# Kernel tuning notes

Measured on AMD Instinct MI355X. Metric: run time of the kernel, lower is better.

Reference implementation:

```python
import jax, jax.numpy as jnp
import numpy as np

ALPHA = 0.0005
TAU = 0.2


def setup_inputs() -> dict:
    key = jax.random.key(0)
    k1, k2, k3 = jax.random.split(key, 3)
    output = jax.random.normal(k1, (8192, 1000), dtype=jnp.float32)
    target = jax.random.normal(k2, (8192, 1000), dtype=jnp.float32)
    conv_w = jax.random.normal(k3, (256, 256, 128, 3), dtype=jnp.float32)
    return {"output": output, "target": target, "conv_w": conv_w}


def reference(output, target, conv_w):
    # base loss (nn.MSELoss with default 'mean' reduction)
    loss = jnp.mean((output - target) ** 2)

    # Diversity regularizer: pairwise cosine similarity between slices
    # conv_w[:, :, i, :] along dim 2 ('filters' = size(2) in the original).
    F = conv_w.shape[2]
    # V: [F, D] with D = out_ch * in_ch * kw
    V = jnp.transpose(conv_w, (2, 0, 1, 3)).reshape(F, -1)
    norms = jnp.linalg.norm(V, axis=1)                      # [F]
    G = (V @ V.T) / (norms[:, None] * norms[None, :])       # [F, F] cosine Gram

    # keep entries with tau < sim <= 1 and i != j
    offdiag = ~jnp.eye(F, dtype=bool)
    mask = (G > TAU) & (G <= 1.0) & offdiag
    reg = jnp.sum(jnp.where(mask, G, jnp.zeros((), dtype=G.dtype)))

    return loss + ALPHA * reg
```

## Files before the change

### kernel.cpp

```cpp
#include <hip/hip_runtime.h>
#include <hip/hip_bf16.h>


typedef __attribute__((ext_vector_type(8))) short bf16x8;
typedef __attribute__((ext_vector_type(4))) float f32x4;

#define ALPHA 0.0005f
#define TAU 0.2f

#define FDIM 128
#define TSTRIDE_DW 52
#define GRAM_NBLK 512
#define CHUNK_F4 3072
#define GRAM_ELEMS (FDIM * FDIM)
#define MSE_N4 2048000
#define MSE_NBLK 2048

__device__ __forceinline__ unsigned int pack_bf2(float lo, float hi) {
    union { float f; unsigned int u; } a, b;
    a.f = lo; b.f = hi;
    unsigned int al = (a.u + 0x7fffu + ((a.u >> 16) & 1u)) >> 16;
    unsigned int bh = (b.u + 0x7fffu + ((b.u >> 16) & 1u)) & 0xffff0000u;
    return (al & 0xffffu) | bh;
}

__global__ void __launch_bounds__(256) mse_kernel(
        const float* __restrict__ o, const float* __restrict__ t,
        float* __restrict__ mse_part) {
    __shared__ float red[4];
    const int tid = threadIdx.x;
    const float4* o4 = reinterpret_cast<const float4*>(o);
    const float4* t4 = reinterpret_cast<const float4*>(t);
    float s = 0.f;
    for (int i = blockIdx.x * 256 + tid; i < MSE_N4; i += MSE_NBLK * 256) {
        float4 a = o4[i], b = t4[i];
        float dx = a.x - b.x, dy = a.y - b.y, dz = a.z - b.z, dw = a.w - b.w;
        s += dx * dx + dy * dy + dz * dz + dw * dw;
    }
    for (int off = 32; off; off >>= 1) s += __shfl_down(s, off);
    if ((tid & 63) == 0) red[tid >> 6] = s;
    __syncthreads();
    if (tid == 0) mse_part[blockIdx.x] = red[0] + red[1] + red[2] + red[3];
}

__device__ __forceinline__ void loadc(const f32x4* __restrict__ src4,
                                      size_t base4, f32x4 (&R)[12]) {
#pragma unroll
    for (int it = 0; it < 6; ++it) {
        R[2 * it]     = src4[base4 + 16 * it];
        R[2 * it + 1] = src4[base4 + 96 + 16 * it];
    }
}

__device__ __forceinline__ void convertc(const f32x4 (&R)[12],
                                         unsigned int* __restrict__ tb,
                                         int p, int q) {
#pragma unroll
    for (int it = 0; it < 6; ++it)
#pragma unroll
        for (int u = 0; u < 4; ++u) {
            const int idx = (q + 16 * it) * 4 + u;
            const int f = idx / 3;
            const int k = idx - 3 * f;
            tb[f * TSTRIDE_DW + k * 16 + p] = pack_bf2(R[2 * it][u], R[2 * it + 1][u]);
        }
}

__device__ __forceinline__ void barrier_tile() {
    asm volatile("s_waitcnt lgkmcnt(0)" ::: "memory");
    __builtin_amdgcn_sched_barrier(0);
    __builtin_amdgcn_s_barrier();
    __builtin_amdgcn_sched_barrier(0);
}

__device__ __forceinline__ void mfmaph(const unsigned short* __restrict__ tu,
                                       int wave, int colr, int hi8,
                                       f32x4 (&acc0)[8], f32x4 (&acc1)[8]) {
#pragma unroll
    for (int ks = 0; ks < 3; ++ks) {
        const int koff = ks * 32 + hi8;
        bf16x8 a0 = *reinterpret_cast<const bf16x8*>(
            &tu[(wave * 32 + colr) * (TSTRIDE_DW * 2) + koff]);
        bf16x8 a1 = *reinterpret_cast<const bf16x8*>(
            &tu[(wave * 32 + 16 + colr) * (TSTRIDE_DW * 2) + koff]);
#pragma unroll
        for (int cc = 0; cc < 8; ++cc) {
            bf16x8 b = *reinterpret_cast<const bf16x8*>(
                &tu[(cc * 16 + colr) * (TSTRIDE_DW * 2) + koff]);
            acc0[cc] = __builtin_amdgcn_mfma_f32_16x16x32_bf16(a0, b, acc0[cc], 0, 0, 0);
            acc1[cc] = __builtin_amdgcn_mfma_f32_16x16x32_bf16(a1, b, acc1[cc], 0, 0, 0);
        }
    }
}

template <int ATOMIC>
__global__ void __launch_bounds__(256, 2) gram_kernel(
        const float* __restrict__ conv, float* __restrict__ out) {
    __shared__ unsigned int tile[2][FDIM * TSTRIDE_DW];
    const int tid = threadIdx.x;
    const int lane = tid & 63;
    const int wave = tid >> 6;
    const int p = tid >> 4;
    const int q = tid & 15;
    const int colr = lane & 15;
    const int hi8 = (lane >> 4) * 8;
    const unsigned short* t0u = reinterpret_cast<const unsigned short*>(tile[0]);
    const unsigned short* t1u = reinterpret_cast<const unsigned short*>(tile[1]);

    f32x4 acc0[8], acc1[8];
#pragma unroll
    for (int cc = 0; cc < 8; ++cc) { acc0[cc] = (f32x4)0.f; acc1[cc] = (f32x4)0.f; }

    const f32x4* src4 = reinterpret_cast<const f32x4*>(conv);
    const size_t cb = (size_t)blockIdx.x * (4 * CHUNK_F4) + (2 * p) * 96 + q;

    f32x4 RA[12], RB[12];
    loadc(src4, cb + 0 * CHUNK_F4, RA);

    loadc(src4, cb + 1 * CHUNK_F4, RB);
    convertc(RA, tile[0], p, q);
    barrier_tile();
    mfmaph(t0u, wave, colr, hi8, acc0, acc1);
    loadc(src4, cb + 2 * CHUNK_F4, RA);
    convertc(RB, tile[1], p, q);
    barrier_tile();
    mfmaph(t1u, wave, colr, hi8, acc0, acc1);
    loadc(src4, cb + 3 * CHUNK_F4, RB);
    convertc(RA, tile[0], p, q);
    barrier_tile();
    mfmaph(t0u, wave, colr, hi8, acc0, acc1);
    convertc(RB, tile[1], p, q);
    barrier_tile();
    mfmaph(t1u, wave, colr, hi8, acc0, acc1);

    float* my = ATOMIC ? out : out + (size_t)blockIdx.x * GRAM_ELEMS;
    const int rsub = (lane >> 4) << 2;
#pragma unroll
    for (int cc = 0; cc < 8; ++cc) {
        const int col = cc * 16 + colr;
#pragma unroll
        for (int j = 0; j < 4; ++j) {
            const int r0 = wave * 32 + rsub + j;
            if (ATOMIC) {
                atomicAdd(&my[r0 * FDIM + col], acc0[cc][j]);
                atomicAdd(&my[(r0 + 16) * FDIM + col], acc1[cc][j]);
            } else {
                my[r0 * FDIM + col] = acc0[cc][j];
                my[(r0 + 16) * FDIM + col] = acc1[cc][j];
            }
        }
    }
}

__global__ void __launch_bounds__(256) reduce_kernel(
        const float* __restrict__ partials, float* __restrict__ gram) {
    __shared__ float acc_s[64][5];
    const int tid = threadIdx.x;
    const int el = tid & 63;
    const int sl = tid >> 6;
    const int e = blockIdx.x * 64 + el;
    float s = 0.f;
#pragma unroll 16
    for (int b = sl * 128; b < sl * 128 + 128; ++b)
        s += partials[(size_t)b * GRAM_ELEMS + e];
    acc_s[el][sl] = s;
    __syncthreads();
    if (tid < 64)
        gram[blockIdx.x * 64 + tid] =
            acc_s[tid][0] + acc_s[tid][1] + acc_s[tid][2] + acc_s[tid][3];
}

__global__ void __launch_bounds__(256) finalize_kernel(
        const float* __restrict__ gram, const float* __restrict__ mse_part,
        float* __restrict__ out) {
    __shared__ float rn[FDIM];
    __shared__ float red[4];
    __shared__ float redm[4];
    const int tid = threadIdx.x;
    if (tid < FDIM) rn[tid] = rsqrtf(gram[tid * (FDIM + 1)]);
    __syncthreads();
    float s = 0.f;
    for (int i = tid; i < GRAM_ELEMS; i += 256) {
        const int row = i >> 7, col = i & 127;
        const float g = gram[i] * rn[row] * rn[col];
        if (row != col && g > TAU && g <= 1.0f) s += g;
    }
    float m = 0.f;
#pragma unroll 8
    for (int j = 0; j < 8; ++j) m += mse_part[tid * 8 + j];
    for (int off = 32; off; off >>= 1) {
        s += __shfl_down(s, off);
        m += __shfl_down(m, off);
    }
    if ((tid & 63) == 0) { red[tid >> 6] = s; redm[tid >> 6] = m; }
    __syncthreads();
    if (tid == 0)
        out[0] = (redm[0] + redm[1] + redm[2] + redm[3]) * (1.0f / 8192000.0f) +
                 ALPHA * (red[0] + red[1] + red[2] + red[3]);
}

extern "C" void kernel_launch(void* const* d_in, const int* in_sizes, int n_in,
                              void* d_out, int out_size, void* d_ws, size_t ws_size,
                              hipStream_t stream) {
    const float* output = (const float*)d_in[0];
    const float* target = (const float*)d_in[1];
    const float* conv   = (const float*)d_in[2];
    float* out = (float*)d_out;

    float* wsf      = (float*)d_ws;
    float* mse_part = wsf;
    float* gram     = wsf + MSE_NBLK;
    float* partials = wsf + MSE_NBLK + GRAM_ELEMS;

    const size_t need =
        (MSE_NBLK + GRAM_ELEMS + (size_t)GRAM_NBLK * GRAM_ELEMS) * sizeof(float);

    if (ws_size >= need) {
        gram_kernel<0><<<GRAM_NBLK, 256, 0, stream>>>(conv, partials);
        mse_kernel<<<MSE_NBLK, 256, 0, stream>>>(output, target, mse_part);
        reduce_kernel<<<GRAM_ELEMS / 64, 256, 0, stream>>>(partials, gram);
    } else {
        hipMemsetAsync(gram, 0, GRAM_ELEMS * sizeof(float), stream);
        gram_kernel<1><<<GRAM_NBLK, 256, 0, stream>>>(conv, gram);
        mse_kernel<<<MSE_NBLK, 256, 0, stream>>>(output, target, mse_part);
    }
    finalize_kernel<<<1, 256, 0, stream>>>(gram, mse_part, out);
}
```

Before: 62.03 us.

## Store Gram partials as packed bf16 pairs to halve partial traffic

Each Gram block now packs its 512 partial 128x128 tiles into bf16 pairs (two rows per 32-bit word) instead of full fp32, halving the partial write and reduce read volume. The reduce kernel unpacks and sums the pairs, and finalize remaps indices to the new packed layout. A sched_barrier is added after the global loads, and the atomic fallback path and workspace size check are removed. This adds rounding error to each partial and assumes a large enough workspace.

```diff
diff --git a/kernel.cpp b/kernel.cpp
--- a/kernel.cpp
+++ b/kernel.cpp
@@ -9,10 +9,11 @@
 #define TAU 0.2f
 
 #define FDIM 128
-#define TSTRIDE_DW 52
+#define TSTRIDE 52
 #define GRAM_NBLK 512
 #define CHUNK_F4 3072
-#define GRAM_ELEMS (FDIM * FDIM)
+#define GRAM_ELEMS 16384
+#define NPAIRQ 8192
 #define MSE_N4 2048000
 #define MSE_NBLK 2048
 
@@ -50,6 +51,7 @@
         R[2 * it]     = src4[base4 + 16 * it];
         R[2 * it + 1] = src4[base4 + 96 + 16 * it];
     }
+    __builtin_amdgcn_sched_barrier(0);
 }
 
 __device__ __forceinline__ void convertc(const f32x4 (&R)[12],
@@ -62,7 +64,7 @@
             const int idx = (q + 16 * it) * 4 + u;
             const int f = idx / 3;
             const int k = idx - 3 * f;
-            tb[f * TSTRIDE_DW + k * 16 + p] = pack_bf2(R[2 * it][u], R[2 * it + 1][u]);
+            tb[f * TSTRIDE + k * 16 + p] = pack_bf2(R[2 * it][u], R[2 * it + 1][u]);
         }
 }
 
@@ -80,23 +82,22 @@
     for (int ks = 0; ks < 3; ++ks) {
         const int koff = ks * 32 + hi8;
         bf16x8 a0 = *reinterpret_cast<const bf16x8*>(
-            &tu[(wave * 32 + colr) * (TSTRIDE_DW * 2) + koff]);
+            &tu[(wave * 32 + colr) * (TSTRIDE * 2) + koff]);
         bf16x8 a1 = *reinterpret_cast<const bf16x8*>(
-            &tu[(wave * 32 + 16 + colr) * (TSTRIDE_DW * 2) + koff]);
+            &tu[(wave * 32 + 16 + colr) * (TSTRIDE * 2) + koff]);
 #pragma unroll
         for (int cc = 0; cc < 8; ++cc) {
             bf16x8 b = *reinterpret_cast<const bf16x8*>(
-                &tu[(cc * 16 + colr) * (TSTRIDE_DW * 2) + koff]);
+                &tu[(cc * 16 + colr) * (TSTRIDE * 2) + koff]);
             acc0[cc] = __builtin_amdgcn_mfma_f32_16x16x32_bf16(a0, b, acc0[cc], 0, 0, 0);
             acc1[cc] = __builtin_amdgcn_mfma_f32_16x16x32_bf16(a1, b, acc1[cc], 0, 0, 0);
         }
     }
 }
 
-template <int ATOMIC>
 __global__ void __launch_bounds__(256, 2) gram_kernel(
-        const float* __restrict__ conv, float* __restrict__ out) {
-    __shared__ unsigned int tile[2][FDIM * TSTRIDE_DW];
+        const float* __restrict__ conv, unsigned int* __restrict__ pp) {
+    __shared__ unsigned int tile[2][FDIM * TSTRIDE];
     const int tid = threadIdx.x;
     const int lane = tid & 63;
     const int wave = tid >> 6;
@@ -133,55 +134,64 @@
     barrier_tile();
     mfmaph(t1u, wave, colr, hi8, acc0, acc1);
 
-    float* my = ATOMIC ? out : out + (size_t)blockIdx.x * GRAM_ELEMS;
+    unsigned int* myp = pp + (size_t)blockIdx.x * NPAIRQ;
     const int rsub = (lane >> 4) << 2;
 #pragma unroll
     for (int cc = 0; cc < 8; ++cc) {
         const int col = cc * 16 + colr;
 #pragma unroll
         for (int j = 0; j < 4; ++j) {
-            const int r0 = wave * 32 + rsub + j;
-            if (ATOMIC) {
-                atomicAdd(&my[r0 * FDIM + col], acc0[cc][j]);
-                atomicAdd(&my[(r0 + 16) * FDIM + col], acc1[cc][j]);
-            } else {
-                my[r0 * FDIM + col] = acc0[cc][j];
-                my[(r0 + 16) * FDIM + col] = acc1[cc][j];
-            }
+            const int pr = wave * 16 + rsub + j;
+            myp[pr * FDIM + col] = pack_bf2(acc0[cc][j], acc1[cc][j]);
         }
     }
 }
 
 __global__ void __launch_bounds__(256) reduce_kernel(
-        const float* __restrict__ partials, float* __restrict__ gram) {
-    __shared__ float acc_s[64][5];
-    const int tid = threadIdx.x;
-    const int el = tid & 63;
-    const int sl = tid >> 6;
-    const int e = blockIdx.x * 64 + el;
-    float s = 0.f;
-#pragma unroll 16
-    for (int b = sl * 128; b < sl * 128 + 128; ++b)
-        s += partials[(size_t)b * GRAM_ELEMS + e];
-    acc_s[el][sl] = s;
-    __syncthreads();
-    if (tid < 64)
-        gram[blockIdx.x * 64 + tid] =
-            acc_s[tid][0] + acc_s[tid][1] + acc_s[tid][2] + acc_s[tid][3];
+        const unsigned int* __restrict__ pp, float* __restrict__ gram) {
+    __shared__ float red[16][16][2];
+    const int tid = threadIdx.x;
+    const int u = tid & 15;
+    const int s = tid >> 4;
+    const int qq = blockIdx.x * 16 + u;
+    float lo = 0.f, hi = 0.f;
+#pragma unroll 8
+    for (int b = s * 32; b < s * 32 + 32; ++b) {
+        const unsigned int v = pp[(size_t)b * NPAIRQ + qq];
+        lo += __uint_as_float(v << 16);
+        hi += __uint_as_float(v & 0xffff0000u);
+    }
+    red[s][u][0] = lo; red[s][u][1] = hi;
+    __syncthreads();
+    if (tid < 32) {
+        const int u2 = tid >> 1, h = tid & 1;
+        float x = 0.f;
+#pragma unroll
+        for (int s2 = 0; s2 < 16; ++s2) x += red[s2][u2][h];
+        gram[(blockIdx.x * 16 + u2) * 2 + h] = x;
+    }
 }
 
 __global__ void __launch_bounds__(256) finalize_kernel(
         const float* __restrict__ gram, const float* __restrict__ mse_part,
         float* __restrict__ out) {
     __shared__ float rn[FDIM];
-    __shared__ float red[4];
-    __shared__ float redm[4];
-    const int tid = threadIdx.x;
-    if (tid < FDIM) rn[tid] = rsqrtf(gram[tid * (FDIM + 1)]);
+    __shared__ float redS[4], redM[4];
+    const int tid = threadIdx.x;
+    if (tid < FDIM) {
+        const int row = tid;
+        const int pr = (row >> 5) * 16 + (row & 15);
+        const int h = (row >> 4) & 1;
+        rn[row] = rsqrtf(gram[(pr * FDIM + row) * 2 + h]);
+    }
     __syncthreads();
     float s = 0.f;
     for (int i = tid; i < GRAM_ELEMS; i += 256) {
-        const int row = i >> 7, col = i & 127;
+        const int h = i & 1;
+        const int qq = i >> 1;
+        const int col = qq & 127;
+        const int pr = qq >> 7;
+        const int row = (pr >> 4) * 32 + (pr & 15) + (h << 4);
         const float g = gram[i] * rn[row] * rn[col];
         if (row != col && g > TAU && g <= 1.0f) s += g;
     }
@@ -192,11 +202,11 @@
         s += __shfl_down(s, off);
         m += __shfl_down(m, off);
     }
-    if ((tid & 63) == 0) { red[tid >> 6] = s; redm[tid >> 6] = m; }
+    if ((tid & 63) == 0) { redS[tid >> 6] = s; redM[tid >> 6] = m; }
     __syncthreads();
     if (tid == 0)
-        out[0] = (redm[0] + redm[1] + redm[2] + redm[3]) * (1.0f / 8192000.0f) +
-                 ALPHA * (red[0] + red[1] + red[2] + red[3]);
+        out[0] = (redM[0] + redM[1] + redM[2] + redM[3]) * (1.0f / 8192000.0f) +
+                 ALPHA * (redS[0] + redS[1] + redS[2] + redS[3]);
 }
 
 extern "C" void kernel_launch(void* const* d_in, const int* in_sizes, int n_in,
@@ -207,22 +217,14 @@
     const float* conv   = (const float*)d_in[2];
     float* out = (float*)d_out;
 
-    float* wsf      = (float*)d_ws;
-    float* mse_part = wsf;
-    float* gram     = wsf + MSE_NBLK;
-    float* partials = wsf + MSE_NBLK + GRAM_ELEMS;
-
-    const size_t need =
-        (MSE_NBLK + GRAM_ELEMS + (size_t)GRAM_NBLK * GRAM_ELEMS) * sizeof(float);
-
-    if (ws_size >= need) {
-        gram_kernel<0><<<GRAM_NBLK, 256, 0, stream>>>(conv, partials);
-        mse_kernel<<<MSE_NBLK, 256, 0, stream>>>(output, target, mse_part);
-        reduce_kernel<<<GRAM_ELEMS / 64, 256, 0, stream>>>(partials, gram);
-    } else {
-        hipMemsetAsync(gram, 0, GRAM_ELEMS * sizeof(float), stream);
-        gram_kernel<1><<<GRAM_NBLK, 256, 0, stream>>>(conv, gram);
-        mse_kernel<<<MSE_NBLK, 256, 0, stream>>>(output, target, mse_part);
-    }
+    float* wsf       = (float*)d_ws;
+    float* mse_part  = wsf;
+    float* gram      = wsf + MSE_NBLK;
+    unsigned int* pp = (unsigned int*)(wsf + MSE_NBLK + GRAM_ELEMS);
+    (void)ws_size;
+
+    gram_kernel<<<GRAM_NBLK, 256, 0, stream>>>(conv, pp);
+    mse_kernel<<<MSE_NBLK, 256, 0, stream>>>(output, target, mse_part);
+    reduce_kernel<<<NPAIRQ / 16, 256, 0, stream>>>(pp, gram);
     finalize_kernel<<<1, 256, 0, stream>>>(gram, mse_part, out);
 }
```

After: 60.88 us. About the same (-1.9%).
